# Kernel optimization log

Measured on AMD Instinct MI355X. Metric: run time of the kernel, lower is better.

Reference implementation:

```python
import jax, jax.numpy as jnp
import numpy as np

D = 1024
B, S = 4, 2048

def setup_inputs() -> dict:
    key = jax.random.key(0)
    ks = jax.random.split(key, 4)
    scale = 1.0 / np.sqrt(D)
    return {
        "x": jax.random.normal(ks[0], (B, S, D), dtype=jnp.float32),
        "Wq": jax.random.normal(ks[1], (D, D), dtype=jnp.float32) * scale,
        "bq": jnp.zeros((D,), jnp.float32),
        "Wk": jax.random.normal(ks[2], (D, D), dtype=jnp.float32) * scale,
        "bk": jnp.zeros((D,), jnp.float32),
        "Wv": jax.random.normal(ks[3], (D, D), dtype=jnp.float32) * scale,
        "bv": jnp.zeros((D,), jnp.float32),
    }

def reference(x, Wq, bq, Wk, bk, Wv, bv):
    # torch Linear: y = x @ W.T + b
    Q = jnp.einsum('bsd,ed->bse', x, Wq) + bq
    K = jnp.einsum('bsd,ed->bse', x, Wk) + bk
    V = jnp.einsum('bsd,ed->bse', x, Wv) + bv
    # NOTE: original scales by sqrt(K.shape[1]) == sqrt(seq_len), kept faithfully
    dk = K.shape[1]
    logits = jnp.einsum('bqd,bkd->bqk', Q, K) / jnp.sqrt(jnp.asarray(dk, Q.dtype))
    att = jax.nn.softmax(logits, axis=-1)
    return jnp.einsum('bqk,bkd->bqd', att, V)
```

## Files before the change

kernel.cpp:

```cpp
#include <hip/hip_runtime.h>


typedef unsigned short u16;
typedef unsigned int u32;
typedef __bf16 bf16x8 __attribute__((ext_vector_type(8)));
typedef float floatx4 __attribute__((ext_vector_type(4)));

__device__ __forceinline__ u16 f2bf(float f) {
    u32 u = __float_as_uint(f);
    u += 0x7fffu + ((u >> 16) & 1u);
    return (u16)(u >> 16);
}

__device__ __forceinline__ void g2lds16(const void* g, void* l) {
    __builtin_amdgcn_global_load_lds(
        (const __attribute__((address_space(1))) unsigned int*)g,
        (__attribute__((address_space(3))) unsigned int*)l,
        16, 0, 0);
}

__global__ __launch_bounds__(256)
void cvt_all(const float* __restrict__ x, const float* __restrict__ Wq,
             const float* __restrict__ Wk, const float* __restrict__ Wv,
             u16* __restrict__ xb, u16* __restrict__ wall,
             float* __restrict__ rowsum)
{
    const int NX = 2097152;
    const int NW = 262144;
    const int TOT = NX + 3 * NW;
    int i = blockIdx.x * 256 + threadIdx.x;
    if (i >= TOT) {
        int z = i - TOT;
        float4 zz = {0.f, 0.f, 0.f, 0.f};
        ((float4*)rowsum)[z] = zz;
        return;
    }
    const float* src;
    u16* dst;
    int idx;
    if (i < NX) { src = x; dst = xb; idx = i; }
    else {
        int j = i - NX;
        dst = wall; idx = j;
        src = (j < NW) ? Wq : (j < 2 * NW) ? Wk : Wv;
        int jj = (j < NW) ? j : (j < 2 * NW) ? (j - NW) : (j - 2 * NW);
        float4 v = ((const float4*)src)[jj];
        ushort4 o;
        o.x = f2bf(v.x); o.y = f2bf(v.y); o.z = f2bf(v.z); o.w = f2bf(v.w);
        ((ushort4*)dst)[idx] = o;
        return;
    }
    float4 v = ((const float4*)src)[idx];
    ushort4 o;
    o.x = f2bf(v.x); o.y = f2bf(v.y); o.z = f2bf(v.z); o.w = f2bf(v.w);
    ((ushort4*)dst)[idx] = o;
}

template<int MODE>
__global__ __launch_bounds__(256)
void gemm_bt(const u16* __restrict__ A, const u16* __restrict__ B,
             void* __restrict__ Out, const float* __restrict__ bias,
             float scale, int M, int N, int K,
             long long sAz, long long sBz, long long sOz,
             void* __restrict__ Out2, void* __restrict__ Out3,
             const float* __restrict__ bias2, const float* __restrict__ bias3,
             float* __restrict__ rowsum)
{
    __shared__ u16 ldsA[2][128 * 64];
    __shared__ u16 ldsB[2][128 * 64];

    const int tid   = threadIdx.x;
    const int lane  = tid & 63;
    const int wv    = tid >> 6;
    const int wm    = (wv >> 1) * 64;
    const int wn    = (wv & 1) * 64;
    const int lhalf = lane & 15;
    const int quad  = lane >> 4;

    const size_t bz = blockIdx.z;
    A += bz * (size_t)sAz;
    B += bz * (size_t)sBz;

    int tm, tn;
    {
        const int ntn = gridDim.x, ntm = gridDim.y;
        const int lin = blockIdx.y * ntn + blockIdx.x;
        const int GM = 4;
        const int width = GM * ntn;
        const int group = lin / width;
        const int first = group * GM;
        const int gsz   = (ntm - first) < GM ? (ntm - first) : GM;
        const int rem   = lin - group * width;
        tm = first + rem % gsz;
        tn = rem / gsz;
    }
    const int m0 = tm * 128;
    const int n0 = tn * 128;

    const int r8 = lane >> 3;
    const int gc = (lane & 7) ^ r8;
    const u16* pa = A + (size_t)(m0 + wv * 32 + r8) * K + gc * 8;
    const u16* pb = B + (size_t)(n0 + wv * 32 + r8) * K + gc * 8;
    const int lofs = wv * 2048;

    floatx4 zero = {0.f, 0.f, 0.f, 0.f};
    floatx4 acc[4][4];
#pragma unroll
    for (int i = 0; i < 4; ++i)
#pragma unroll
        for (int j = 0; j < 4; ++j) acc[i][j] = zero;

    const int swz = lhalf & 7;

#pragma unroll
    for (int j = 0; j < 4; ++j) {
        g2lds16(pa + (size_t)(j * 8) * K, &ldsA[0][lofs + j * 512]);
        g2lds16(pb + (size_t)(j * 8) * K, &ldsB[0][lofs + j * 512]);
    }
    pa += 64; pb += 64;

    int buf = 0;
    for (int k0 = 0; k0 < K; k0 += 64) {
        __syncthreads();
        if (k0 + 64 < K) {
#pragma unroll
            for (int j = 0; j < 4; ++j) {
                g2lds16(pa + (size_t)(j * 8) * K, &ldsA[buf ^ 1][lofs + j * 512]);
                g2lds16(pb + (size_t)(j * 8) * K, &ldsB[buf ^ 1][lofs + j * 512]);
            }
            pa += 64; pb += 64;
        }

        const u16* lA = ldsA[buf];
        const u16* lB = ldsB[buf];
#pragma unroll
        for (int ks = 0; ks < 2; ++ks) {
            const int c = ks * 4 + quad;
            const int p = c ^ swz;
            bf16x8 af[4], bfv[4];
#pragma unroll
            for (int i = 0; i < 4; ++i)
                af[i] = *(const bf16x8*)(lA + (wm + i * 16 + lhalf) * 64 + p * 8);
#pragma unroll
            for (int j = 0; j < 4; ++j)
                bfv[j] = *(const bf16x8*)(lB + (wn + j * 16 + lhalf) * 64 + p * 8);
#pragma unroll
            for (int i = 0; i < 4; ++i)
#pragma unroll
                for (int j = 0; j < 4; ++j)
                    acc[i][j] = __builtin_amdgcn_mfma_f32_16x16x32_bf16(
                        af[i], bfv[j], acc[i][j], 0, 0, 0);
        }
        buf ^= 1;
    }

#pragma unroll
    for (int i = 0; i < 4; ++i) {
        const int mb = m0 + wm + i * 16 + quad * 4;
        if (MODE == 3) {
#pragma unroll
            for (int j = 0; j < 4; ++j) {
                const int n = n0 + wn + j * 16 + lhalf;
                if (n < 1024) {
                    const float bb = bias[n];
#pragma unroll
                    for (int r = 0; r < 4; ++r)
                        ((u16*)Out)[(size_t)(mb + r) * 1024 + n] =
                            f2bf(acc[i][j][r] + bb);
                } else if (n < 2048) {
                    const float bb = bias2[n - 1024];
#pragma unroll
                    for (int r = 0; r < 4; ++r)
                        ((u16*)Out2)[(size_t)(mb + r) * 1024 + (n - 1024)] =
                            f2bf(acc[i][j][r] + bb);
                } else {
                    const int d = n - 2048;
                    const float bb = bias3[d];
                    const int b = mb >> 11;
                    const int s0 = mb & 2047;
                    ushort4 w;
                    w.x = f2bf(acc[i][j][0] + bb);
                    w.y = f2bf(acc[i][j][1] + bb);
                    w.z = f2bf(acc[i][j][2] + bb);
                    w.w = f2bf(acc[i][j][3] + bb);
                    *(ushort4*)((u16*)Out3 + (size_t)b * 2097152 +
                                (size_t)d * 2048 + s0) = w;
                }
            }
        } else if (MODE == 4) {
#pragma unroll
            for (int r = 0; r < 4; ++r) {
                const int m = mb + r;
                float rs = 0.f;
#pragma unroll
                for (int j = 0; j < 4; ++j) {
                    const int n = n0 + wn + j * 16 + lhalf;
                    const float e = __expf(acc[i][j][r] * scale);
                    ((u16*)Out)[bz * (size_t)sOz + (size_t)m * N + n] = f2bf(e);
                    rs += e;
                }
                rs += __shfl_xor(rs, 1, 64);
                rs += __shfl_xor(rs, 2, 64);
                rs += __shfl_xor(rs, 4, 64);
                rs += __shfl_xor(rs, 8, 64);
                if (lhalf == 0)
                    atomicAdd(&rowsum[bz * 2048 + m], rs);
            }
        } else {
            float4 rs4 = *(const float4*)&rowsum[bz * 2048 + mb];
            float rinv[4];
            rinv[0] = __builtin_amdgcn_rcpf(rs4.x);
            rinv[1] = __builtin_amdgcn_rcpf(rs4.y);
            rinv[2] = __builtin_amdgcn_rcpf(rs4.z);
            rinv[3] = __builtin_amdgcn_rcpf(rs4.w);
#pragma unroll
            for (int j = 0; j < 4; ++j) {
                const int n = n0 + wn + j * 16 + lhalf;
#pragma unroll
                for (int r = 0; r < 4; ++r)
                    ((float*)Out)[bz * (size_t)sOz + (size_t)(mb + r) * N + n] =
                        acc[i][j][r] * rinv[r];
            }
        }
    }
}

extern "C" void kernel_launch(void* const* d_in, const int* in_sizes, int n_in,
                              void* d_out, int out_size, void* d_ws, size_t ws_size,
                              hipStream_t stream)
{
    const float* x  = (const float*)d_in[0];
    const float* Wq = (const float*)d_in[1];
    const float* bq = (const float*)d_in[2];
    const float* Wk = (const float*)d_in[3];
    const float* bk = (const float*)d_in[4];
    const float* Wv = (const float*)d_in[5];
    const float* bv = (const float*)d_in[6];
    float* out = (float*)d_out;

    const int B = 4, S = 2048, D = 1024;
    const long long SD = (long long)S * D;
    const long long SS = (long long)S * S;
    const long long BSD = (long long)B * SD;
    const long long DD = (long long)D * D;

    u16* xb   = (u16*)d_ws;
    u16* wall = xb   + BSD;
    u16* Qb   = wall + 3 * DD;
    u16* Kb   = Qb   + BSD;
    u16* Vt   = Kb   + BSD;
    u16* Sc   = Vt   + BSD;
    float* rowsum = (float*)(Sc + B * SS);

    cvt_all<<<dim3(11272), 256, 0, stream>>>(x, Wq, Wk, Wv, xb, wall, rowsum);

    gemm_bt<3><<<dim3(3 * D / 128, (B * S) / 128, 1), 256, 0, stream>>>(
        xb, wall, Qb, bq, 1.f, B * S, 3 * D, D, 0, 0, 0,
        Kb, Vt, bk, bv, nullptr);

    const float sc = 0.022097086912079608f;
    gemm_bt<4><<<dim3(S / 128, S / 128, B), 256, 0, stream>>>(
        Qb, Kb, Sc, nullptr, sc, S, S, D, SD, SD, SS,
        nullptr, nullptr, nullptr, nullptr, rowsum);

    gemm_bt<5><<<dim3(D / 128, S / 128, B), 256, 0, stream>>>(
        Sc, Vt, out, nullptr, 1.f, S, D, S, SS, SD, SD,
        nullptr, nullptr, nullptr, nullptr, rowsum);
}
```

Measured before the change: 252.0 us.

## Add 256x256-tile 8-wave GEMM with quadrant pipelining for QKV and scores

Introduces a new GEMM kernel with 512 threads and 256x256 output tiles. The tile is split into quadrants whose LDS loads, global-to-LDS prefetches and MFMA batches are interleaved across barriers, with setprio around the MFMAs. The kernel replaces the 128x128 GEMM for the fused QKV projection and the QK^T score/exp stage. The aim is more data reuse per loaded tile and better overlap of memory with compute. In exchange it uses a larger LDS footprint, higher register pressure and fewer blocks, which may hurt occupancy and tail balance.

```diff
diff --git a/kernel.cpp b/kernel.cpp
--- a/kernel.cpp
+++ b/kernel.cpp
@@ -225,6 +225,233 @@
     }
 }
 
+template<int MODE>
+__global__ __launch_bounds__(512, 2)
+void gemm8p(const u16* __restrict__ A, const u16* __restrict__ B,
+            void* __restrict__ Out, const float* __restrict__ bias,
+            float scale, int M, int N, int K,
+            long long sAz, long long sBz, long long sOz,
+            void* __restrict__ Out2, void* __restrict__ Out3,
+            const float* __restrict__ bias2, const float* __restrict__ bias3,
+            float* __restrict__ rowsum)
+{
+    __shared__ u16 lds[2][2][2][8192];
+
+    const int tid   = threadIdx.x;
+    const int lane  = tid & 63;
+    const int wv    = tid >> 6;
+    const int wr    = wv >> 2;
+    const int wc    = wv & 3;
+    const int lhalf = lane & 15;
+    const int quad  = lane >> 4;
+    const int swz   = lhalf & 7;
+
+    const size_t bz = blockIdx.z;
+    A += bz * (size_t)sAz;
+    B += bz * (size_t)sBz;
+
+    int tm, tn;
+    {
+        const int ntn = gridDim.x, ntm = gridDim.y;
+        const int lin = blockIdx.y * ntn + blockIdx.x;
+        const int GM = 4;
+        const int width = GM * ntn;
+        const int group = lin / width;
+        const int first = group * GM;
+        const int gsz   = (ntm - first) < GM ? (ntm - first) : GM;
+        const int rem   = lin - group * width;
+        tm = first + rem % gsz;
+        tn = rem / gsz;
+    }
+    const int m0 = tm * 256;
+    const int n0 = tn * 256;
+
+    const int r8l = lane >> 3;
+    const int gc  = (lane & 7) ^ r8l;
+    const u16* pA = A + (size_t)(m0 + wv * 8 + r8l) * K + gc * 8;
+    const u16* pB = B + (size_t)(n0 + wv * 8 + r8l) * K + gc * 8;
+    const int wofs = wv * 512;
+
+    const int NT = K >> 6;
+
+#define STAGE8(op, slot, half, kt) do {                                        \
+    const u16* _s = ((op) ? pB : pA) + (size_t)((half) * 128) * K              \
+                    + (size_t)(kt) * 64;                                       \
+    u16* _d = &lds[slot][op][half][wofs];                                      \
+    g2lds16(_s, _d);                                                           \
+    g2lds16(_s + (size_t)64 * K, _d + 4096);                                   \
+} while (0)
+
+    bf16x8 af[2][4];
+    bf16x8 bfr[2][2][2];
+    floatx4 zero = {0.f, 0.f, 0.f, 0.f};
+    floatx4 acc[2][2][4][2];
+#pragma unroll
+    for (int a = 0; a < 2; ++a)
+#pragma unroll
+    for (int b = 0; b < 2; ++b)
+#pragma unroll
+    for (int i = 0; i < 4; ++i)
+#pragma unroll
+    for (int j = 0; j < 2; ++j) acc[a][b][i][j] = zero;
+
+#define LDA8(slot, qm) do {                                                    \
+    const u16* _a = &lds[slot][0][qm][0];                                      \
+    _Pragma("unroll")                                                          \
+    for (int ks = 0; ks < 2; ++ks) {                                           \
+        const int p8 = ((ks * 4 + quad) ^ swz) * 8;                            \
+        _Pragma("unroll")                                                      \
+        for (int i = 0; i < 4; ++i)                                            \
+            af[ks][i] = *(const bf16x8*)(_a + (wr * 64 + i * 16 + lhalf) * 64  \
+                                         + p8);                                \
+    }                                                                          \
+} while (0)
+
+#define LDB8(slot, qn) do {                                                    \
+    const u16* _b = &lds[slot][1][qn][0];                                      \
+    _Pragma("unroll")                                                          \
+    for (int ks = 0; ks < 2; ++ks) {                                           \
+        const int p8 = ((ks * 4 + quad) ^ swz) * 8;                            \
+        _Pragma("unroll")                                                      \
+        for (int j = 0; j < 2; ++j)                                            \
+            bfr[qn][ks][j] = *(const bf16x8*)(_b +                             \
+                (wc * 32 + j * 16 + lhalf) * 64 + p8);                         \
+    }                                                                          \
+} while (0)
+
+#define MFMAQ(qm, qn) do {                                                     \
+    _Pragma("unroll")                                                          \
+    for (int ks = 0; ks < 2; ++ks)                                             \
+        _Pragma("unroll")                                                      \
+        for (int i = 0; i < 4; ++i)                                            \
+            _Pragma("unroll")                                                  \
+            for (int j = 0; j < 2; ++j)                                        \
+                acc[qm][qn][i][j] = __builtin_amdgcn_mfma_f32_16x16x32_bf16(   \
+                    af[ks][i], bfr[qn][ks][j], acc[qm][qn][i][j], 0, 0, 0);    \
+} while (0)
+
+    STAGE8(0, 0, 0, 0);
+    STAGE8(1, 0, 0, 0);
+    STAGE8(0, 0, 1, 0);
+    STAGE8(1, 0, 1, 0);
+    if (NT > 1) {
+        STAGE8(0, 1, 0, 1);
+        STAGE8(1, 1, 0, 1);
+    }
+    asm volatile("s_waitcnt vmcnt(4)");
+    __builtin_amdgcn_s_barrier();
+
+    for (int t = 0; t < NT; ++t) {
+        const int s = t & 1;
+        const bool p1 = (t + 1 < NT), p2 = (t + 2 < NT);
+
+        LDA8(s, 0);
+        LDB8(s, 0);
+        if (p1) STAGE8(0, s ^ 1, 1, t + 1);
+        __builtin_amdgcn_s_barrier();
+        asm volatile("s_waitcnt lgkmcnt(0)");
+        __builtin_amdgcn_s_setprio(1);
+        MFMAQ(0, 0);
+        __builtin_amdgcn_s_setprio(0);
+        __builtin_amdgcn_s_barrier();
+
+        LDB8(s, 1);
+        if (p1) STAGE8(1, s ^ 1, 1, t + 1);
+        __builtin_amdgcn_s_barrier();
+        asm volatile("s_waitcnt lgkmcnt(0)");
+        __builtin_amdgcn_s_setprio(1);
+        MFMAQ(0, 1);
+        __builtin_amdgcn_s_setprio(0);
+        __builtin_amdgcn_s_barrier();
+
+        LDA8(s, 1);
+        if (p2) STAGE8(0, s, 0, t + 2);
+        __builtin_amdgcn_s_barrier();
+        asm volatile("s_waitcnt lgkmcnt(0)");
+        __builtin_amdgcn_s_setprio(1);
+        MFMAQ(1, 0);
+        __builtin_amdgcn_s_setprio(0);
+        __builtin_amdgcn_s_barrier();
+
+        if (p2) STAGE8(1, s, 0, t + 2);
+        __builtin_amdgcn_s_barrier();
+        asm volatile("s_waitcnt lgkmcnt(0)");
+        __builtin_amdgcn_s_setprio(1);
+        MFMAQ(1, 1);
+        __builtin_amdgcn_s_setprio(0);
+        if (p2) asm volatile("s_waitcnt vmcnt(4)");
+        else    asm volatile("s_waitcnt vmcnt(0)");
+        __builtin_amdgcn_s_barrier();
+    }
+
+#undef STAGE8
+#undef LDA8
+#undef LDB8
+#undef MFMAQ
+
+#pragma unroll
+    for (int qm = 0; qm < 2; ++qm)
+#pragma unroll
+    for (int i = 0; i < 4; ++i) {
+        const int mb = m0 + qm * 128 + wr * 64 + i * 16 + quad * 4;
+        if (MODE == 3) {
+#pragma unroll
+            for (int qn = 0; qn < 2; ++qn)
+#pragma unroll
+            for (int j = 0; j < 2; ++j) {
+                const int n = n0 + qn * 128 + wc * 32 + j * 16 + lhalf;
+                const floatx4 a = acc[qm][qn][i][j];
+                if (n < 1024) {
+                    const float bb = bias[n];
+#pragma unroll
+                    for (int r = 0; r < 4; ++r)
+                        ((u16*)Out)[(size_t)(mb + r) * 1024 + n] =
+                            f2bf(a[r] + bb);
+                } else if (n < 2048) {
+                    const float bb = bias2[n - 1024];
+#pragma unroll
+                    for (int r = 0; r < 4; ++r)
+                        ((u16*)Out2)[(size_t)(mb + r) * 1024 + (n - 1024)] =
+                            f2bf(a[r] + bb);
+                } else {
+                    const int d = n - 2048;
+                    const float bb = bias3[d];
+                    const int b = mb >> 11;
+                    const int s0 = mb & 2047;
+                    ushort4 w;
+                    w.x = f2bf(a[0] + bb);
+                    w.y = f2bf(a[1] + bb);
+                    w.z = f2bf(a[2] + bb);
+                    w.w = f2bf(a[3] + bb);
+                    *(ushort4*)((u16*)Out3 + (size_t)b * 2097152 +
+                                (size_t)d * 2048 + s0) = w;
+                }
+            }
+        } else {
+#pragma unroll
+            for (int r = 0; r < 4; ++r) {
+                const int m = mb + r;
+                float rs = 0.f;
+#pragma unroll
+                for (int qn = 0; qn < 2; ++qn)
+#pragma unroll
+                for (int j = 0; j < 2; ++j) {
+                    const int n = n0 + qn * 128 + wc * 32 + j * 16 + lhalf;
+                    const float e = __expf(acc[qm][qn][i][j][r] * scale);
+                    ((u16*)Out)[bz * (size_t)sOz + (size_t)m * N + n] = f2bf(e);
+                    rs += e;
+                }
+                rs += __shfl_xor(rs, 1, 64);
+                rs += __shfl_xor(rs, 2, 64);
+                rs += __shfl_xor(rs, 4, 64);
+                rs += __shfl_xor(rs, 8, 64);
+                if (lhalf == 0)
+                    atomicAdd(&rowsum[bz * 2048 + m], rs);
+            }
+        }
+    }
+}
+
 extern "C" void kernel_launch(void* const* d_in, const int* in_sizes, int n_in,
                               void* d_out, int out_size, void* d_ws, size_t ws_size,
                               hipStream_t stream)
@@ -254,12 +481,12 @@
 
     cvt_all<<<dim3(11272), 256, 0, stream>>>(x, Wq, Wk, Wv, xb, wall, rowsum);
 
-    gemm_bt<3><<<dim3(3 * D / 128, (B * S) / 128, 1), 256, 0, stream>>>(
+    gemm8p<3><<<dim3(3 * D / 256, (B * S) / 256, 1), 512, 0, stream>>>(
         xb, wall, Qb, bq, 1.f, B * S, 3 * D, D, 0, 0, 0,
         Kb, Vt, bk, bv, nullptr);
 
     const float sc = 0.022097086912079608f;
-    gemm_bt<4><<<dim3(S / 128, S / 128, B), 256, 0, stream>>>(
+    gemm8p<4><<<dim3(S / 256, S / 256, B), 512, 0, stream>>>(
         Qb, Kb, Sc, nullptr, sc, S, S, D, SD, SD, SS,
         nullptr, nullptr, nullptr, nullptr, rowsum);
 
```

Measured after the change: 255.8 us. Within noise of the previous version (+1.5%).
